# Kernel optimization log

Hardware: AMD Instinct MI355X
Metric: run time of the kernel (lower is better)

Reference implementation:

```python
import jax, jax.numpy as jnp
import numpy as np

RANK = 8
NUM_MORPH = 10000   # morpheme vocab (num_embeddings)
CORE_DIM = 8        # ceil(512 ** (1/3))
ORDER = 3
NUM_SURF = 50000    # word vocab (num_surfaces)
EMB_DIM = 512
LN_EPS = 1e-5
BATCH, SEQ = 8, 2048


def setup_inputs() -> dict:
    key = jax.random.key(0)
    kx, kc, kw = jax.random.split(key, 3)
    # token ids over the word vocabulary
    x = jax.random.randint(kx, (BATCH, SEQ), 0, NUM_SURF, dtype=jnp.int64)
    # word -> morpheme-id mapping, one id per tensor-train order position
    co_matrix = jax.random.randint(kc, (NUM_SURF, ORDER), 0, NUM_MORPH, dtype=jnp.int64)
    # xavier_uniform over (rank, num_morph, core_dim): fan_in = num_morph*core_dim, fan_out = rank*core_dim
    bound = float(np.sqrt(6.0 / (NUM_MORPH * CORE_DIM + RANK * CORE_DIM)))
    weight = jax.random.uniform(kw, (RANK, NUM_MORPH, CORE_DIM), dtype=jnp.float32,
                                minval=-bound, maxval=bound)
    weight = weight.at[:, 0].set(0.0)  # reset_parameters zeroes morpheme index 0
    ln_scale = jnp.ones((EMB_DIM,), dtype=jnp.float32)
    ln_bias = jnp.zeros((EMB_DIM,), dtype=jnp.float32)
    return {"x": x, "co_matrix": co_matrix, "weight": weight,
            "ln_scale": ln_scale, "ln_bias": ln_bias}


def _emb_matrix(weight, co_matrix, ln_scale, ln_bias):
    # gather all order cores at once: [rank, num_surf, order, core_dim]
    cores = weight[:, co_matrix, :]
    w = cores[:, :, 0, :]                                  # [R, S, C]
    for i in range(1, ORDER):
        # order-wise broadcast outer product, flattened feature dim grows C^i
        w = (w[:, :, :, None] * cores[:, :, i, None, :]).reshape(RANK, NUM_SURF, -1)
    w = w.sum(axis=0)[:, :EMB_DIM]                         # [S, EMB_DIM]
    mu = jnp.mean(w, axis=-1, keepdims=True)
    var = jnp.var(w, axis=-1, keepdims=True)
    return (w - mu) * jax.lax.rsqrt(var + LN_EPS) * ln_scale + ln_bias


def reference(x, co_matrix, weight, ln_scale, ln_bias):
    emb = _emb_matrix(weight, co_matrix, ln_scale, ln_bias)  # full-vocab table
    return emb[x]                                            # [B, S, EMB_DIM]
```

## Files before the change

kernel.cpp:

```cpp
#include <hip/hip_runtime.h>


#define RANK      8
#define NUM_MORPH 10000
#define EMB       512
#define LN_EPS    1e-5f
#define WPB       4
#define RSTRIDE   80000

typedef float f32x4 __attribute__((ext_vector_type(4)));

template <int CTRL>
__device__ __forceinline__ float dpp_add(float v) {
    return v + __int_as_float(__builtin_amdgcn_update_dpp(
        __float_as_int(v), __float_as_int(v), CTRL, 0xf, 0xf, false));
}
__device__ __forceinline__ float rdlane(float v, int l) {
    return __int_as_float(__builtin_amdgcn_readlane(__float_as_int(v), l));
}

__global__ __launch_bounds__(256) void morph_emb_kernel(
    const int* __restrict__ x,
    const int* __restrict__ co,
    const float* __restrict__ W,
    const float* __restrict__ lns,
    const float* __restrict__ lnb,
    float* __restrict__ out,
    int n_tok) {
    const int lane = threadIdx.x & 63;
    const int wid  = blockIdx.x * WPB + (threadIdx.x >> 6);
    const int tok  = (wid < n_tok) ? wid : (n_tok - 1);

    const int s  = x[tok];
    const int m0 = co[s * 3 + 0];
    const int m1 = co[s * 3 + 1];
    const int m2 = co[s * 3 + 2];

    const float c_mine =
        W[(size_t)(lane >> 3) * RSTRIDE + (size_t)m2 * 8 + (lane & 7)];

    const float* pa = W + (size_t)m0 * 8 + (lane >> 3);
    const float* pb = W + (size_t)m1 * 8 + (lane & 7);
    float p[RANK];
#pragma unroll
    for (int r = 0; r < RANK; ++r)
        p[r] = pa[r * RSTRIDE] * pb[r * RSTRIDE];

    const int e = lane << 3;
    const f32x4 g0 = *reinterpret_cast<const f32x4*>(lns + e);
    const f32x4 g1 = *reinterpret_cast<const f32x4*>(lns + e + 4);
    const f32x4 b0 = *reinterpret_cast<const f32x4*>(lnb + e);
    const f32x4 b1 = *reinterpret_cast<const f32x4*>(lnb + e + 4);

    float acc[8] = {0.f, 0.f, 0.f, 0.f, 0.f, 0.f, 0.f, 0.f};
#pragma unroll
    for (int r = 0; r < RANK; ++r) {
#pragma unroll
        for (int j = 0; j < 8; ++j)
            acc[j] = fmaf(p[r], rdlane(c_mine, r * 8 + j), acc[j]);
    }

    float sm = 0.f, sq = 0.f;
#pragma unroll
    for (int j = 0; j < 8; ++j) { sm += acc[j]; sq += acc[j] * acc[j]; }
    sm = dpp_add<0xB1>(sm);  sq = dpp_add<0xB1>(sq);
    sm = dpp_add<0x4E>(sm);  sq = dpp_add<0x4E>(sq);
    sm = dpp_add<0x141>(sm); sq = dpp_add<0x141>(sq);
    sm = dpp_add<0x140>(sm); sq = dpp_add<0x140>(sq);
    const float tot_s = (rdlane(sm, 0) + rdlane(sm, 16)) +
                        (rdlane(sm, 32) + rdlane(sm, 48));
    const float tot_q = (rdlane(sq, 0) + rdlane(sq, 16)) +
                        (rdlane(sq, 32) + rdlane(sq, 48));
    const float mu = tot_s * (1.0f / EMB);
    const float rs = rsqrtf(tot_q * (1.0f / EMB) - mu * mu + LN_EPS);

    if (wid < n_tok) {
        f32x4 o0, o1;
        o0[0] = (acc[0] - mu) * rs * g0[0] + b0[0];
        o0[1] = (acc[1] - mu) * rs * g0[1] + b0[1];
        o0[2] = (acc[2] - mu) * rs * g0[2] + b0[2];
        o0[3] = (acc[3] - mu) * rs * g0[3] + b0[3];
        o1[0] = (acc[4] - mu) * rs * g1[0] + b1[0];
        o1[1] = (acc[5] - mu) * rs * g1[1] + b1[1];
        o1[2] = (acc[6] - mu) * rs * g1[2] + b1[2];
        o1[3] = (acc[7] - mu) * rs * g1[3] + b1[3];
        f32x4* op = reinterpret_cast<f32x4*>(out + (size_t)wid * EMB + e);
        __builtin_nontemporal_store(o0, op);
        __builtin_nontemporal_store(o1, op + 1);
    }
}

extern "C" void kernel_launch(void* const* d_in, const int* in_sizes, int n_in,
                              void* d_out, int out_size, void* d_ws, size_t ws_size,
                              hipStream_t stream) {
    const int*   x   = (const int*)d_in[0];
    const int*   co  = (const int*)d_in[1];
    const float* W   = (const float*)d_in[2];
    const float* lns = (const float*)d_in[3];
    const float* lnb = (const float*)d_in[4];
    float*       out = (float*)d_out;

    const int n_tok  = in_sizes[0];
    const int blocks = (n_tok + WPB - 1) / WPB;
    morph_emb_kernel<<<blocks, WPB * 64, 0, stream>>>(x, co, W, lns, lnb, out, n_tok);
}
```

Measured before the change: 16.61 us.

## Transpose weight to morpheme-major layout and gather cores via ds_bpermute

Adds a pre-pass kernel that rearranges the weight tensor into a morpheme-major layout in workspace, with all ranks and core dims contiguous as 64 floats per morpheme. The main kernel then loads each of the three cores with a single coalesced 256-byte load and builds the rank-wise products with ds_bpermute, replacing 16 scattered strided gathers per lane. The goal is fewer scattered memory transactions per token. In exchange it adds an extra kernel launch and a full transpose of the 2.5 MB weight on every call. The old path is kept as a fallback when the workspace is too small.

Measured after the change: 19.25 us. 15.9% more time.

```diff
diff --git a/kernel.cpp b/kernel.cpp
--- a/kernel.cpp
+++ b/kernel.cpp
@@ -7,6 +7,7 @@
 #define LN_EPS    1e-5f
 #define WPB       4
 #define RSTRIDE   80000
+#define W_ELEMS   (RANK * NUM_MORPH * 8)
 
 typedef float f32x4 __attribute__((ext_vector_type(4)));
 
@@ -18,11 +19,27 @@
 __device__ __forceinline__ float rdlane(float v, int l) {
     return __int_as_float(__builtin_amdgcn_readlane(__float_as_int(v), l));
 }
+__device__ __forceinline__ float bperm(int byte_addr, float v) {
+    return __int_as_float(__builtin_amdgcn_ds_bpermute(byte_addr, __float_as_int(v)));
+}
 
+__global__ __launch_bounds__(256) void transpose_w(
+    const float* __restrict__ W, float* __restrict__ Wt) {
+    const int lane = threadIdx.x & 63;
+    const int wv   = threadIdx.x >> 6;
+    const int m    = blockIdx.x * 32 + wv * 8 + (lane >> 3);
+    const int d    = lane & 7;
+    if (m >= NUM_MORPH) return;
+#pragma unroll
+    for (int r = 0; r < RANK; ++r)
+        Wt[m * 64 + r * 8 + d] = W[r * RSTRIDE + m * 8 + d];
+}
+
+template <bool TRANSPOSED>
 __global__ __launch_bounds__(256) void morph_emb_kernel(
     const int* __restrict__ x,
     const int* __restrict__ co,
-    const float* __restrict__ W,
+    const float* __restrict__ Wp,
     const float* __restrict__ lns,
     const float* __restrict__ lnb,
     float* __restrict__ out,
@@ -36,15 +53,25 @@
     const int m1 = co[s * 3 + 1];
     const int m2 = co[s * 3 + 2];
 
-    const float c_mine =
-        W[(size_t)(lane >> 3) * RSTRIDE + (size_t)m2 * 8 + (lane & 7)];
-
-    const float* pa = W + (size_t)m0 * 8 + (lane >> 3);
-    const float* pb = W + (size_t)m1 * 8 + (lane & 7);
     float p[RANK];
+    float c_mine;
+    if (TRANSPOSED) {
+        const float a_vec = Wp[m0 * 64 + lane];
+        const float b_vec = Wp[m1 * 64 + lane];
+        c_mine            = Wp[m2 * 64 + lane];
+        const int a4 = (lane >> 3) << 2;
+        const int b4 = (lane & 7) << 2;
 #pragma unroll
-    for (int r = 0; r < RANK; ++r)
-        p[r] = pa[r * RSTRIDE] * pb[r * RSTRIDE];
+        for (int r = 0; r < RANK; ++r)
+            p[r] = bperm(a4 + r * 32, a_vec) * bperm(b4 + r * 32, b_vec);
+    } else {
+        c_mine = Wp[(size_t)(lane >> 3) * RSTRIDE + (size_t)m2 * 8 + (lane & 7)];
+        const float* pa = Wp + (size_t)m0 * 8 + (lane >> 3);
+        const float* pb = Wp + (size_t)m1 * 8 + (lane & 7);
+#pragma unroll
+        for (int r = 0; r < RANK; ++r)
+            p[r] = pa[r * RSTRIDE] * pb[r * RSTRIDE];
+    }
 
     const int e = lane << 3;
     const f32x4 g0 = *reinterpret_cast<const f32x4*>(lns + e);
@@ -102,5 +129,14 @@
 
     const int n_tok  = in_sizes[0];
     const int blocks = (n_tok + WPB - 1) / WPB;
-    morph_emb_kernel<<<blocks, WPB * 64, 0, stream>>>(x, co, W, lns, lnb, out, n_tok);
+
+    if (ws_size >= (size_t)W_ELEMS * sizeof(float)) {
+        float* Wt = (float*)d_ws;
+        transpose_w<<<(NUM_MORPH + 31) / 32, 256, 0, stream>>>(W, Wt);
+        morph_emb_kernel<true><<<blocks, WPB * 64, 0, stream>>>(
+            x, co, Wt, lns, lnb, out, n_tok);
+    } else {
+        morph_emb_kernel<false><<<blocks, WPB * 64, 0, stream>>>(
+            x, co, W, lns, lnb, out, n_tok);
+    }
 }
```

## Process four tokens per wave and load cores via one coalesced gather plus bpermute

Applied to the files above, without the earlier changes.

Each wavefront now handles four tokens instead of one, with a quarter as many blocks launched. All core loads use a single per-lane gather (rank x core_dim across the 64 lanes) for each of the three morphemes. The per-rank factors for the first two cores are broadcast with ds_bpermute rather than loaded redundantly by every lane. The goal is fewer global load instructions, more memory-level parallelism per wave, and amortised launch and LN setup cost. In exchange it raises register pressure, lowers wave count, and adds LDS-path permutes.

After: 14.41 us. 1.15x faster.

```diff
diff --git a/kernel.cpp b/kernel.cpp
--- a/kernel.cpp
+++ b/kernel.cpp
@@ -6,6 +6,7 @@
 #define EMB       512
 #define LN_EPS    1e-5f
 #define WPB       4
+#define TPW       4
 #define RSTRIDE   80000
 
 typedef float f32x4 __attribute__((ext_vector_type(4)));
@@ -18,6 +19,9 @@
 __device__ __forceinline__ float rdlane(float v, int l) {
     return __int_as_float(__builtin_amdgcn_readlane(__float_as_int(v), l));
 }
+__device__ __forceinline__ float bperm(int byte_addr, float v) {
+    return __int_as_float(__builtin_amdgcn_ds_bpermute(byte_addr, __float_as_int(v)));
+}
 
 __global__ __launch_bounds__(256) void morph_emb_kernel(
     const int* __restrict__ x,
@@ -29,22 +33,31 @@
     int n_tok) {
     const int lane = threadIdx.x & 63;
     const int wid  = blockIdx.x * WPB + (threadIdx.x >> 6);
-    const int tok  = (wid < n_tok) ? wid : (n_tok - 1);
+    const int t0   = wid * TPW;
 
-    const int s  = x[tok];
-    const int m0 = co[s * 3 + 0];
-    const int m1 = co[s * 3 + 1];
-    const int m2 = co[s * 3 + 2];
+    const int r_ln = lane >> 3;
+    const int d_ln = lane & 7;
+    const size_t gofs = (size_t)r_ln * RSTRIDE + d_ln;
 
-    const float c_mine =
-        W[(size_t)(lane >> 3) * RSTRIDE + (size_t)m2 * 8 + (lane & 7)];
-
-    const float* pa = W + (size_t)m0 * 8 + (lane >> 3);
-    const float* pb = W + (size_t)m1 * 8 + (lane & 7);
-    float p[RANK];
+    int s_[TPW], m0_[TPW], m1_[TPW], m2_[TPW];
 #pragma unroll
-    for (int r = 0; r < RANK; ++r)
-        p[r] = pa[r * RSTRIDE] * pb[r * RSTRIDE];
+    for (int t = 0; t < TPW; ++t) {
+        int tt = t0 + t; if (tt >= n_tok) tt = n_tok - 1;
+        s_[t]  = x[tt];
+    }
+#pragma unroll
+    for (int t = 0; t < TPW; ++t) {
+        m0_[t] = co[s_[t] * 3 + 0];
+        m1_[t] = co[s_[t] * 3 + 1];
+        m2_[t] = co[s_[t] * 3 + 2];
+    }
+    float am[TPW], bm[TPW], cm[TPW];
+#pragma unroll
+    for (int t = 0; t < TPW; ++t) {
+        am[t] = W[gofs + (size_t)m0_[t] * 8];
+        bm[t] = W[gofs + (size_t)m1_[t] * 8];
+        cm[t] = W[gofs + (size_t)m2_[t] * 8];
+    }
 
     const int e = lane << 3;
     const f32x4 g0 = *reinterpret_cast<const f32x4*>(lns + e);
@@ -52,41 +65,59 @@
     const f32x4 b0 = *reinterpret_cast<const f32x4*>(lnb + e);
     const f32x4 b1 = *reinterpret_cast<const f32x4*>(lnb + e + 4);
 
-    float acc[8] = {0.f, 0.f, 0.f, 0.f, 0.f, 0.f, 0.f, 0.f};
+    const int aaddr = r_ln << 2;
+    const int baddr = d_ln << 2;
+    float acc[TPW][8] = {};
 #pragma unroll
     for (int r = 0; r < RANK; ++r) {
 #pragma unroll
-        for (int j = 0; j < 8; ++j)
-            acc[j] = fmaf(p[r], rdlane(c_mine, r * 8 + j), acc[j]);
+        for (int t = 0; t < TPW; ++t) {
+            const float p = bperm(aaddr + r * 32, am[t]) *
+                            bperm(baddr + r * 32, bm[t]);
+#pragma unroll
+            for (int j = 0; j < 8; ++j)
+                acc[t][j] = fmaf(p, rdlane(cm[t], r * 8 + j), acc[t][j]);
+        }
     }
 
-    float sm = 0.f, sq = 0.f;
+    float sm[TPW], sq[TPW];
 #pragma unroll
-    for (int j = 0; j < 8; ++j) { sm += acc[j]; sq += acc[j] * acc[j]; }
-    sm = dpp_add<0xB1>(sm);  sq = dpp_add<0xB1>(sq);
-    sm = dpp_add<0x4E>(sm);  sq = dpp_add<0x4E>(sq);
-    sm = dpp_add<0x141>(sm); sq = dpp_add<0x141>(sq);
-    sm = dpp_add<0x140>(sm); sq = dpp_add<0x140>(sq);
-    const float tot_s = (rdlane(sm, 0) + rdlane(sm, 16)) +
-                        (rdlane(sm, 32) + rdlane(sm, 48));
-    const float tot_q = (rdlane(sq, 0) + rdlane(sq, 16)) +
-                        (rdlane(sq, 32) + rdlane(sq, 48));
-    const float mu = tot_s * (1.0f / EMB);
-    const float rs = rsqrtf(tot_q * (1.0f / EMB) - mu * mu + LN_EPS);
+    for (int t = 0; t < TPW; ++t) {
+        float s = 0.f, q = 0.f;
+#pragma unroll
+        for (int j = 0; j < 8; ++j) { s += acc[t][j]; q += acc[t][j] * acc[t][j]; }
+        sm[t] = s; sq[t] = q;
+    }
+#pragma unroll
+    for (int t = 0; t < TPW; ++t) {
+        sm[t] = dpp_add<0xB1>(sm[t]);  sq[t] = dpp_add<0xB1>(sq[t]);
+        sm[t] = dpp_add<0x4E>(sm[t]);  sq[t] = dpp_add<0x4E>(sq[t]);
+        sm[t] = dpp_add<0x141>(sm[t]); sq[t] = dpp_add<0x141>(sq[t]);
+        sm[t] = dpp_add<0x140>(sm[t]); sq[t] = dpp_add<0x140>(sq[t]);
+    }
 
-    if (wid < n_tok) {
-        f32x4 o0, o1;
-        o0[0] = (acc[0] - mu) * rs * g0[0] + b0[0];
-        o0[1] = (acc[1] - mu) * rs * g0[1] + b0[1];
-        o0[2] = (acc[2] - mu) * rs * g0[2] + b0[2];
-        o0[3] = (acc[3] - mu) * rs * g0[3] + b0[3];
-        o1[0] = (acc[4] - mu) * rs * g1[0] + b1[0];
-        o1[1] = (acc[5] - mu) * rs * g1[1] + b1[1];
-        o1[2] = (acc[6] - mu) * rs * g1[2] + b1[2];
-        o1[3] = (acc[7] - mu) * rs * g1[3] + b1[3];
-        f32x4* op = reinterpret_cast<f32x4*>(out + (size_t)wid * EMB + e);
-        __builtin_nontemporal_store(o0, op);
-        __builtin_nontemporal_store(o1, op + 1);
+#pragma unroll
+    for (int t = 0; t < TPW; ++t) {
+        const float ts = (rdlane(sm[t], 0) + rdlane(sm[t], 16)) +
+                         (rdlane(sm[t], 32) + rdlane(sm[t], 48));
+        const float tq = (rdlane(sq[t], 0) + rdlane(sq[t], 16)) +
+                         (rdlane(sq[t], 32) + rdlane(sq[t], 48));
+        const float mu = ts * (1.0f / EMB);
+        const float rs = rsqrtf(tq * (1.0f / EMB) - mu * mu + LN_EPS);
+        if (t0 + t < n_tok) {
+            f32x4 o0, o1;
+            o0[0] = (acc[t][0] - mu) * rs * g0[0] + b0[0];
+            o0[1] = (acc[t][1] - mu) * rs * g0[1] + b0[1];
+            o0[2] = (acc[t][2] - mu) * rs * g0[2] + b0[2];
+            o0[3] = (acc[t][3] - mu) * rs * g0[3] + b0[3];
+            o1[0] = (acc[t][4] - mu) * rs * g1[0] + b1[0];
+            o1[1] = (acc[t][5] - mu) * rs * g1[1] + b1[1];
+            o1[2] = (acc[t][6] - mu) * rs * g1[2] + b1[2];
+            o1[3] = (acc[t][7] - mu) * rs * g1[3] + b1[3];
+            f32x4* op = reinterpret_cast<f32x4*>(out + (size_t)(t0 + t) * EMB + e);
+            __builtin_nontemporal_store(o0, op);
+            __builtin_nontemporal_store(o1, op + 1);
+        }
     }
 }
 
@@ -100,7 +131,8 @@
     const float* lnb = (const float*)d_in[4];
     float*       out = (float*)d_out;
 
-    const int n_tok  = in_sizes[0];
-    const int blocks = (n_tok + WPB - 1) / WPB;
+    const int n_tok = in_sizes[0];
+    const int tok_per_block = WPB * TPW;
+    const int blocks = (n_tok + tok_per_block - 1) / tok_per_block;
     morph_emb_kernel<<<blocks, WPB * 64, 0, stream>>>(x, co, W, lns, lnb, out, n_tok);
 }
```
